# Kernel tuning notes

Measured on AMD Instinct MI355X. Metric: run time of the kernel, lower is better.

## Reference

```python
import jax, jax.numpy as jnp
import numpy as np

N, C, H, W = 4, 256, 32, 32
NH = 2                      # att_nhead
HD = C // NH                # 128 per-head dim
MAX_DIS = 7
WS = 2 * MAX_DIS + 1        # 15 window side
WW = WS * WS                # 225 window positions
T = (C / NH) ** 0.5


def _gather_idx(h, w):
    # idx[wpos, m]: flat index into zero-padded (h+14, w+14) grid of the
    # neighbor at window offset wpos for query pixel m (== F.unfold semantics)
    pw = w + 2 * MAX_DIS
    dy, dx = np.meshgrid(np.arange(WS), np.arange(WS), indexing='ij')
    ys, xs = np.meshgrid(np.arange(h), np.arange(w), indexing='ij')
    idx = (dy.reshape(-1, 1) + ys.reshape(1, -1)) * pw + (dx.reshape(-1, 1) + xs.reshape(1, -1))
    return jnp.asarray(idx, dtype=jnp.int32)  # [WW, h*w]


def setup_inputs() -> dict:
    key = jax.random.key(0)
    ks = jax.random.split(key, 14)
    s = 0.02
    return {
        'q': jax.random.normal(ks[0], (N, C, H, W), jnp.float32),
        'k': jax.random.normal(ks[1], (N, C, H, W), jnp.float32),
        'v': jax.random.normal(ks[2], (N, C, H, W), jnp.float32),
        'Wq': jax.random.normal(ks[3], (C, C), jnp.float32) * s,
        'bq': jnp.zeros((C,), jnp.float32),
        'Wk': jax.random.normal(ks[4], (C, C), jnp.float32) * s,
        'bk': jnp.zeros((C,), jnp.float32),
        'Wv': jax.random.normal(ks[5], (C, C), jnp.float32) * s,
        'bv': jnp.zeros((C,), jnp.float32),
        'Wrel': jax.random.normal(ks[6], (NH, WW, HD), jnp.float32) * s,   # grouped 1x1 conv
        'brel': jnp.zeros((NH * WW,), jnp.float32),
        'V_bias': jax.random.normal(ks[7], (NH, HD, WW), jnp.float32) * s,
        'Wfc': jax.random.normal(ks[8], (C, C), jnp.float32) * s,
        'bfc': jnp.zeros((C,), jnp.float32),
    }


def _conv1x1(x, Wt, b):
    return jnp.einsum('nchw,dc->ndhw', x, Wt) + b[None, :, None, None]


def reference(q, k, v, Wq, bq, Wk, bk, Wv, bv, Wrel, brel, V_bias, Wfc, bfc):
    n, c, h, w = q.shape
    hw = h * w
    idx = _gather_idx(h, w)                                   # [WW, hw]
    pad = ((0, 0), (0, 0), (0, 0), (MAX_DIS, MAX_DIS), (MAX_DIS, MAX_DIS))

    q = _conv1x1(q, Wq, bq)
    k = _conv1x1(k, Wk, bk)
    v = _conv1x1(v, Wv, bv)

    # grouped 1x1 conv: relative position logits, [n, NH, WW, hw]
    rel = jnp.einsum('ngcxy,gwc->ngwxy', q.reshape(n, NH, HD, h, w), Wrel)
    rel = rel + brel.reshape(NH, WW)[None, :, :, None, None]
    rel = rel.reshape(n, NH, WW, hw)

    qs = (q / T).reshape(n, NH, HD, hw)

    # unfold K via zero-pad + gather: [n, NH, HD, WW, hw]
    k_pad = jnp.pad(k.reshape(n, NH, HD, h, w), pad).reshape(n, NH, HD, -1)
    k_un = k_pad[..., idx]
    qk = jnp.einsum('ngcm,ngcwm->ngwm', qs, k_un) + rel

    # boundary mask: neighbor inside the original image
    valid = jnp.pad(jnp.ones((h, w), jnp.float32), MAX_DIS).reshape(-1)[idx] > 0
    qk = jnp.where(valid[None, None], qk, jnp.float32(-1e8))
    attn = jax.nn.softmax(qk, axis=2)                         # over window positions

    agg_bias = jnp.einsum('ngwm,gcw->mngc', attn, V_bias).reshape(hw, n, c)

    # local2global scatter + dense einsum == gather of zero-padded V
    v_pad = jnp.pad(v.reshape(n, NH, HD, h, w), pad).reshape(n, NH, HD, -1)
    v_un = v_pad[..., idx]                                    # [n, NH, HD, WW, hw]
    agg_value = jnp.einsum('ngwm,ngcwm->mngc', attn, v_un).reshape(hw, n, c)

    out = (agg_value + agg_bias) @ Wfc.T + bfc                # [hw, n, c]
    return out
```

## Files before the change

### kernel.cpp

```cpp
#include <hip/hip_runtime.h>
#include <math.h>


typedef __attribute__((ext_vector_type(8))) short short8;
typedef __attribute__((ext_vector_type(4))) short short4v;
typedef __attribute__((ext_vector_type(4))) float floatx4;

__device__ __forceinline__ short f2bf(float f) {
    unsigned u = __float_as_uint(f);
    unsigned r = (u + 0x7fffu + ((u >> 16) & 1u)) >> 16;
    return (short)r;
}
__device__ __forceinline__ float bf2f(short s) {
    return __uint_as_float(((unsigned)(unsigned short)s) << 16);
}

__global__ __launch_bounds__(256)
void conv_kernel(const float* __restrict__ q, const float* __restrict__ k,
                 const float* __restrict__ v,
                 const float* __restrict__ Wq, const float* __restrict__ Wk,
                 const float* __restrict__ Wv, const float* __restrict__ Wfc,
                 const float* __restrict__ Wrel,
                 short* __restrict__ Xhi, short* __restrict__ Xlo,
                 short* __restrict__ Whi, short* __restrict__ Wlo,
                 short* __restrict__ Wrh, short* __restrict__ Wrl)
{
    const int tid = threadIdx.x;
    const int z = blockIdx.z;
    const int lane = tid & 63;
    const int n16 = lane & 15, quad = lane >> 4;

    if (z < 12) {
        __shared__ float st[64 * 33];
        const int sel = z >> 2, batch = z & 3;
        const float* X = (sel == 0 ? q : sel == 1 ? k : v) + ((long)batch << 18);
        const int mb = blockIdx.x, kc = blockIdx.y;
#pragma unroll
        for (int it = 0; it < 8; ++it) {
            int e = tid + it * 256;
            int cc = e >> 6, mm = e & 63;
            st[mm * 33 + cc] = X[((long)(kc * 32 + cc) << 10) + mb * 64 + mm];
        }
        __syncthreads();
        const int mtl = tid >> 6;
        const int m = mtl * 16 + n16;
        short h[8], l[8];
#pragma unroll
        for (int j = 0; j < 8; ++j) {
            float f = st[m * 33 + quad * 8 + j];
            short hb = f2bf(f);
            h[j] = hb;
            l[j] = f2bf(f - bf2f(hb));
        }
        int mt16 = mb * 4 + mtl;
        long off = (long)z * 262144 + (((long)(mt16 * 8 + kc) * 64) + lane) * 8;
        *(short8*)(Xhi + off) = *(short8*)&h[0];
        *(short8*)(Xlo + off) = *(short8*)&l[0];
    } else if (z < 16) {
        if (tid >= 64) return;
        const int w = z - 12;
        const float* W = (w == 0 ? Wq : w == 1 ? Wk : w == 2 ? Wv : Wfc);
        const int dt = blockIdx.x, kc = blockIdx.y;
        const int d = dt * 16 + n16, cb = kc * 32 + quad * 8;
        float4 w0 = *(const float4*)&W[d * 256 + cb];
        float4 w1 = *(const float4*)&W[d * 256 + cb + 4];
        float f[8] = {w0.x, w0.y, w0.z, w0.w, w1.x, w1.y, w1.z, w1.w};
        short h[8], l[8];
#pragma unroll
        for (int j = 0; j < 8; ++j) {
            short hb = f2bf(f[j]);
            h[j] = hb;
            l[j] = f2bf(f[j] - bf2f(hb));
        }
        long off = (long)w * 65536 + (((long)(dt * 8 + kc) * 64) + lane) * 8;
        *(short8*)(Whi + off) = *(short8*)&h[0];
        *(short8*)(Wlo + off) = *(short8*)&l[0];
    } else {
        if (tid >= 64) return;
        const int g = z - 16;
        const int wt = blockIdx.x, kc = blockIdx.y;
        if (wt >= 15 || kc >= 4) return;
        const int w = wt * 16 + n16;
        const int cb = kc * 32 + quad * 8;
        float f[8] = {0.f, 0.f, 0.f, 0.f, 0.f, 0.f, 0.f, 0.f};
        if (w < 225) {
            float4 w0 = *(const float4*)&Wrel[(long)(g * 225 + w) * 128 + cb];
            float4 w1 = *(const float4*)&Wrel[(long)(g * 225 + w) * 128 + cb + 4];
            f[0] = w0.x; f[1] = w0.y; f[2] = w0.z; f[3] = w0.w;
            f[4] = w1.x; f[5] = w1.y; f[6] = w1.z; f[7] = w1.w;
        }
        short h[8], l[8];
#pragma unroll
        for (int j = 0; j < 8; ++j) {
            short hb = f2bf(f[j]);
            h[j] = hb;
            l[j] = f2bf(f[j] - bf2f(hb));
        }
        long off = (long)g * 30720 + (((long)(wt * 4 + kc) * 64) + lane) * 8;
        *(short8*)(Wrh + off) = *(short8*)&h[0];
        *(short8*)(Wrl + off) = *(short8*)&l[0];
    }
}

__global__ __launch_bounds__(256)
void mfma_proj(const short* __restrict__ Xhi, const short* __restrict__ Xlo,
               const short* __restrict__ Whi, const short* __restrict__ Wlo,
               const float* __restrict__ bq, const float* __restrict__ bk,
               const float* __restrict__ bv,
               short* __restrict__ qhi, short* __restrict__ qlo,
               short* __restrict__ khi, short* __restrict__ klo,
               float* __restrict__ vpad)
{
    __shared__ float tile[16 * 65];
    const int tid = threadIdx.x;
    const int wave = tid >> 6, lane = tid & 63;
    const int n16 = lane & 15, quad = lane >> 4;
    const int mt16 = blockIdx.x, db = blockIdx.y, z = blockIdx.z;
    const int sel = z >> 2, batch = z & 3;
    const int dt = db * 4 + wave;

    const short* Ah = Whi + (long)sel * 65536 + ((long)(dt * 8) * 64 + lane) * 8;
    const short* Al = Wlo + (long)sel * 65536 + ((long)(dt * 8) * 64 + lane) * 8;
    const short* Bh = Xhi + (long)z * 262144;
    const short* Bl = Xlo + (long)z * 262144;

    const float* bias = (sel == 0 ? bq : sel == 1 ? bk : bv);
    float4 bv4 = *(const float4*)&bias[dt * 16 + quad * 4];
    float bb[4] = {bv4.x, bv4.y, bv4.z, bv4.w};

    floatx4 acc = {0.f, 0.f, 0.f, 0.f};
#pragma unroll
    for (int kc = 0; kc < 8; ++kc) {
        short8 ahi = *(const short8*)(Ah + kc * 512);
        short8 alo = *(const short8*)(Al + kc * 512);
        long bo = ((long)(mt16 * 8 + kc) * 64 + lane) * 8;
        short8 bh = *(const short8*)(Bh + bo);
        short8 bl = *(const short8*)(Bl + bo);
        acc = __builtin_amdgcn_mfma_f32_16x16x32_bf16(ahi, bh, acc, 0, 0, 0);
        acc = __builtin_amdgcn_mfma_f32_16x16x32_bf16(ahi, bl, acc, 0, 0, 0);
        acc = __builtin_amdgcn_mfma_f32_16x16x32_bf16(alo, bh, acc, 0, 0, 0);
    }

    if (sel == 2) {
        const int m = mt16 * 16 + n16;
        float* Y = vpad + (long)batch * 393216;
        const int row = m >> 5, col = (m & 31) + 8;
#pragma unroll
        for (int r = 0; r < 4; ++r)
            Y[(long)(dt * 16 + quad * 4 + r) * 1536 + row * 48 + col] = acc[r] + bb[r];
        {
            const int prow = mt16 >> 1, side = mt16 & 1;
            const int ch_l = tid >> 2, f2 = (tid & 3) * 2;
            long po = (long)(db * 64 + ch_l) * 1536 + prow * 48 + side * 40 + f2;
            Y[po] = 0.f;
            Y[po + 1] = 0.f;
        }
        return;
    }

    const int cl = wave * 16 + quad * 4;
#pragma unroll
    for (int r = 0; r < 4; ++r)
        tile[n16 * 65 + cl + r] = acc[r] + bb[r];
    __syncthreads();

    const float scale = (sel == 1) ? 0.08838834764831845f : 1.0f;
    const int m_l = tid >> 4, c16 = (tid & 15) * 4;
    const int m = mt16 * 16 + m_l;
    const int cglob = db * 64 + c16;
    const int g = cglob >> 7, ch = cglob & 127;
    const long base = (((long)(batch * 2 + g) << 10) + m) * 128 + ch;
    short h[4], l[4];
#pragma unroll
    for (int j = 0; j < 4; ++j) {
        float f = tile[m_l * 65 + c16 + j] * scale;
        short hb = f2bf(f);
        h[j] = hb;
        l[j] = f2bf(f - bf2f(hb));
    }
    short* oh = sel ? khi : qhi;
    short* ol = sel ? klo : qlo;
    *(short4v*)(oh + base) = *(short4v*)&h[0];
    *(short4v*)(ol + base) = *(short4v*)&l[0];
}

__global__ __launch_bounds__(256)
void scores_pv(const short* __restrict__ qhi, const short* __restrict__ qlo,
               const short* __restrict__ khi, const short* __restrict__ klo,
               const short* __restrict__ Wrh, const short* __restrict__ Wrl,
               const float* __restrict__ brel,
               const float* __restrict__ vpad, const float* __restrict__ Vbias,
               short* __restrict__ AGhi, short* __restrict__ AGlo)
{
    __shared__ float qk[16 * 241];
    __shared__ float pa2[225 * 16];
    __shared__ float tile[16 * 133];
    __shared__ float invl[16];

    const int tid = threadIdx.x;
    const int wave = tid >> 6, lane = tid & 63;
    const int y  = blockIdx.x >> 1;
    const int xt = blockIdx.x & 1;
    const int bz = blockIdx.y;
    const int g = bz & 1;
    const int x0 = xt * 16;

    const int n16 = lane & 15, quad = lane >> 4;
    const long qbase = (((long)bz << 10) + y * 32 + x0 + n16) * 128 + quad * 8;
    short8 a_hi[4], a_lo[4];
#pragma unroll
    for (int ch = 0; ch < 4; ++ch) {
        a_hi[ch] = *(const short8*)(qhi + qbase + ch * 32);
        a_lo[ch] = *(const short8*)(qlo + qbase + ch * 32);
    }

    for (int wt = wave; wt < 15; wt += 4) {
        const short* Ah = Wrh + (long)g * 30720 + ((long)(wt * 4) * 64 + lane) * 8;
        const short* Al = Wrl + (long)g * 30720 + ((long)(wt * 4) * 64 + lane) * 8;
        floatx4 racc = {0.f, 0.f, 0.f, 0.f};
#pragma unroll
        for (int kc = 0; kc < 4; ++kc) {
            short8 whh = *(const short8*)(Ah + kc * 512);
            short8 wll = *(const short8*)(Al + kc * 512);
            racc = __builtin_amdgcn_mfma_f32_16x16x32_bf16(whh, a_hi[kc], racc, 0, 0, 0);
            racc = __builtin_amdgcn_mfma_f32_16x16x32_bf16(whh, a_lo[kc], racc, 0, 0, 0);
            racc = __builtin_amdgcn_mfma_f32_16x16x32_bf16(wll, a_hi[kc], racc, 0, 0, 0);
        }
#pragma unroll
        for (int r = 0; r < 4; ++r) {
            int w = wt * 16 + quad * 4 + r;
            if (w < 225) {
                int dy = w / 15, dx = w - dy * 15;
                qk[n16 * 241 + dy * 16 + dx] = racc[r] + brel[g * 225 + w];
            }
        }
    }
    __syncthreads();

    for (int e = tid; e < 16 * 241; e += 256) {
        int px = e / 241, idx = e - px * 241;
        int dy = idx >> 4, dx = idx & 15;
        int hy = y + dy - 7, hx = x0 + px + dx - 7;
        bool valid = (dx < 15) && (dy < 15) &&
                     (hy >= 0) && (hy < 32) && (hx >= 0) && (hx < 32);
        if (!valid) qk[e] = -1e8f;
    }
    __syncthreads();

    for (int dy = wave; dy < 15; dy += 4) {
        const int ky = y + dy - 7;
        if (ky < 0 || ky > 31) continue;
#pragma unroll
        for (int kxt = 0; kxt < 2; ++kxt) {
            const int kxg = x0 - 8 + kxt * 16 + n16;
            const long kb = (((long)bz << 10) + ky * 32 + kxg) * 128 + quad * 8;
            floatx4 acc = {0.f, 0.f, 0.f, 0.f};
#pragma unroll
            for (int ch = 0; ch < 4; ++ch) {
                short8 b_hi = *(const short8*)(khi + kb + ch * 32);
                short8 b_lo = *(const short8*)(klo + kb + ch * 32);
                acc = __builtin_amdgcn_mfma_f32_16x16x32_bf16(a_hi[ch], b_hi, acc, 0, 0, 0);
                acc = __builtin_amdgcn_mfma_f32_16x16x32_bf16(a_hi[ch], b_lo, acc, 0, 0, 0);
                acc = __builtin_amdgcn_mfma_f32_16x16x32_bf16(a_lo[ch], b_hi, acc, 0, 0, 0);
            }
            if (kxg >= 0 && kxg < 32) {
#pragma unroll
                for (int r = 0; r < 4; ++r) {
                    int m = quad * 4 + r;
                    int dx = kxg - (x0 + m) + 7;
                    if (dx >= 0 && dx < 15) {
                        int s = m * 241 + dy * 16 + dx;
                        qk[s] = qk[s] + acc[r];
                    }
                }
            }
        }
    }
    __syncthreads();

    {
        int px = tid >> 4, s = tid & 15;
        float mx = -3.0e38f;
        for (int w = s; w < 240; w += 16) mx = fmaxf(mx, qk[px * 241 + w]);
#pragma unroll
        for (int msk = 8; msk; msk >>= 1) mx = fmaxf(mx, __shfl_xor(mx, msk));
        float sum = 0.f;
        for (int w = s; w < 240; w += 16) {
            float p = __expf(qk[px * 241 + w] - mx);
            qk[px * 241 + w] = p;
            sum += p;
        }
#pragma unroll
        for (int msk = 8; msk; msk >>= 1) sum += __shfl_xor(sum, msk);
        if (s == 0) invl[px] = 1.0f / sum;
    }
    __syncthreads();

    for (int e = tid; e < 3600; e += 256) {
        int w = e >> 4, px = e & 15;
        int dy2 = w / 15, dx2 = w - dy2 * 15;
        pa2[w * 16 + px] = qk[px * 241 + dy2 * 16 + dx2] * invl[px];
    }
    __syncthreads();

    const int n = bz >> 1;
    const int chg2 = tid >> 2;
    const int xq   = tid & 3;
    const int c0   = chg2 * 2;
    const int xb   = x0 + xq * 4;
    const float* v0 = vpad + (long)bz * 196608 + (long)c0 * 1536;
    const float* v1 = v0 + 1536;
    const float* b0 = Vbias + (g * 128 + c0) * 225;
    const float* b1 = b0 + 225;

    float acc0[4] = {0.f, 0.f, 0.f, 0.f};
    float acc1[4] = {0.f, 0.f, 0.f, 0.f};

    for (int dy = 0; dy < 15; ++dy) {
        int hy = y + dy - 7;
        if (hy < 0 || hy > 31) continue;
        const float4* r0 = (const float4*)(v0 + hy * 48 + xb);
        const float4* r1 = (const float4*)(v1 + hy * 48 + xb);
        float wa[20], wb[20];
#pragma unroll
        for (int t = 0; t < 5; ++t) {
            float4 a = r0[t], b = r1[t];
            wa[4*t+0] = a.x; wa[4*t+1] = a.y; wa[4*t+2] = a.z; wa[4*t+3] = a.w;
            wb[4*t+0] = b.x; wb[4*t+1] = b.y; wb[4*t+2] = b.z; wb[4*t+3] = b.w;
        }
        const float* par = &pa2[dy * 15 * 16 + xq * 4];
        const float* vb0 = b0 + dy * 15;
        const float* vb1 = b1 + dy * 15;
#pragma unroll
        for (int dx = 0; dx < 15; ++dx) {
            float4 p4 = *(const float4*)&par[dx * 16];
            float ba = vb0[dx], bb = vb1[dx];
            acc0[0] += p4.x * (wa[1 + dx] + ba);
            acc0[1] += p4.y * (wa[2 + dx] + ba);
            acc0[2] += p4.z * (wa[3 + dx] + ba);
            acc0[3] += p4.w * (wa[4 + dx] + ba);
            acc1[0] += p4.x * (wb[1 + dx] + bb);
            acc1[1] += p4.y * (wb[2 + dx] + bb);
            acc1[2] += p4.z * (wb[3 + dx] + bb);
            acc1[3] += p4.w * (wb[4 + dx] + bb);
        }
    }

#pragma unroll
    for (int i = 0; i < 4; ++i) {
        tile[(xq * 4 + i) * 133 + c0 + 0] = acc0[i];
        tile[(xq * 4 + i) * 133 + c0 + 1] = acc1[i];
    }
    __syncthreads();

    const int sub = tid >> 6;
    short h[8], l[8];
#pragma unroll
    for (int j = 0; j < 8; ++j) {
        float f = tile[n16 * 133 + sub * 32 + quad * 8 + j];
        short hb = f2bf(f);
        h[j] = hb;
        l[j] = f2bf(f - bf2f(hb));
    }
    const int mt16 = y * 2 + xt;
    const int kc = g * 4 + sub;
    long off = (long)n * 262144 + (((long)(mt16 * 8 + kc) * 64) + lane) * 8;
    *(short8*)(AGhi + off) = *(short8*)&h[0];
    *(short8*)(AGlo + off) = *(short8*)&l[0];
}

__global__ __launch_bounds__(256)
void mfma_fc(const short* __restrict__ Ahi, const short* __restrict__ Alo,
             const short* __restrict__ Whi, const short* __restrict__ Wlo,
             const float* __restrict__ bfc, float* __restrict__ out)
{
    __shared__ float tile[16 * 68];
    const int tid = threadIdx.x;
    const int wave = tid >> 6, lane = tid & 63;
    const int n16 = lane & 15, quad = lane >> 4;
    const int mt16 = blockIdx.x, db = blockIdx.y, nz = blockIdx.z;
    const int dt = db * 4 + wave;

    const short* Ah = Whi + (long)3 * 65536 + ((long)(dt * 8) * 64 + lane) * 8;
    const short* Al = Wlo + (long)3 * 65536 + ((long)(dt * 8) * 64 + lane) * 8;
    const short* Bh = Ahi + (long)nz * 262144;
    const short* Bl = Alo + (long)nz * 262144;

    float4 bv4 = *(const float4*)&bfc[dt * 16 + quad * 4];
    float bb[4] = {bv4.x, bv4.y, bv4.z, bv4.w};

    floatx4 acc = {0.f, 0.f, 0.f, 0.f};
#pragma unroll
    for (int kc = 0; kc < 8; ++kc) {
        short8 ahi = *(const short8*)(Ah + kc * 512);
        short8 alo = *(const short8*)(Al + kc * 512);
        long bo = ((long)(mt16 * 8 + kc) * 64 + lane) * 8;
        short8 bh = *(const short8*)(Bh + bo);
        short8 bl = *(const short8*)(Bl + bo);
        acc = __builtin_amdgcn_mfma_f32_16x16x32_bf16(ahi, bh, acc, 0, 0, 0);
        acc = __builtin_amdgcn_mfma_f32_16x16x32_bf16(ahi, bl, acc, 0, 0, 0);
        acc = __builtin_amdgcn_mfma_f32_16x16x32_bf16(alo, bh, acc, 0, 0, 0);
    }

    const int dl = wave * 16 + quad * 4;
#pragma unroll
    for (int r = 0; r < 4; ++r)
        tile[n16 * 68 + dl + r] = acc[r] + bb[r];
    __syncthreads();

    const int mm = tid >> 4, d4 = (tid & 15) * 4;
    float4 o4 = *(const float4*)&tile[mm * 68 + d4];
    *(float4*)&out[(long)(mt16 * 16 + mm) * 1024 + nz * 256 + db * 64 + d4] = o4;
}

extern "C" void kernel_launch(void* const* d_in, const int* in_sizes, int n_in,
                              void* d_out, int out_size, void* d_ws, size_t ws_size,
                              hipStream_t stream)
{
    const float* q    = (const float*)d_in[0];
    const float* k    = (const float*)d_in[1];
    const float* v    = (const float*)d_in[2];
    const float* Wq   = (const float*)d_in[3];
    const float* bq   = (const float*)d_in[4];
    const float* Wk   = (const float*)d_in[5];
    const float* bk   = (const float*)d_in[6];
    const float* Wv   = (const float*)d_in[7];
    const float* bv   = (const float*)d_in[8];
    const float* Wrel = (const float*)d_in[9];
    const float* brel = (const float*)d_in[10];
    const float* Vb   = (const float*)d_in[11];
    const float* Wfc  = (const float*)d_in[12];
    const float* bfc  = (const float*)d_in[13];
    float* out = (float*)d_out;

    float* ws   = (float*)d_ws;
    float* vpad = ws + 2097152;
    short* qhi  = (short*)(ws + 6561792);
    short* qlo  = (short*)(ws + 7086080);
    short* khi  = (short*)(ws + 7610368);
    short* klo  = (short*)(ws + 8134656);
    short* Xhi  = (short*)(ws + 8658944);
    short* Xlo  = (short*)(ws + 10231808);
    short* Whi  = (short*)(ws + 11804672);
    short* Wlo  = (short*)(ws + 11935744);
    short* AGhi = (short*)(ws + 12066816);
    short* AGlo = (short*)(ws + 12591104);
    short* Wrh  = (short*)(ws + 13115392);
    short* Wrl  = (short*)(ws + 13146112);

    dim3 blk(256);

    conv_kernel<<<dim3(16, 8, 18), blk, 0, stream>>>(q, k, v, Wq, Wk, Wv, Wfc,
                                                     Wrel, Xhi, Xlo, Whi, Wlo,
                                                     Wrh, Wrl);

    mfma_proj<<<dim3(64, 4, 12), blk, 0, stream>>>(Xhi, Xlo, Whi, Wlo,
                                                   bq, bk, bv,
                                                   qhi, qlo, khi, klo, vpad);

    scores_pv<<<dim3(64, 8), blk, 0, stream>>>(qhi, qlo, khi, klo,
                                               Wrh, Wrl, brel,
                                               vpad, Vb, AGhi, AGlo);

    mfma_fc<<<dim3(64, 4, 4), blk, 0, stream>>>(AGhi, AGlo, Whi, Wlo, bfc, out);
}
```

Baseline: 169.9 us.

## Split scores_pv channel work across two blocks and alias shared memory

Doubles the scores_pv grid from 512 to 1024 blocks by splitting the 128 channels into two halves, each block computing one channel per thread instead of two. The grid is linearized with batch-head fastest. The qk and output tile shared buffers are aliased to cut LDS use and allow more resident blocks. The cost is that the QK scores, relative logits and softmax are now computed twice per pixel tile, once in each channel-half block.

```diff
diff --git a/kernel.cpp b/kernel.cpp
--- a/kernel.cpp
+++ b/kernel.cpp
@@ -192,16 +192,21 @@
                const float* __restrict__ vpad, const float* __restrict__ Vbias,
                short* __restrict__ AGhi, short* __restrict__ AGlo)
 {
-    __shared__ float qk[16 * 241];
-    __shared__ float pa2[225 * 16];
-    __shared__ float tile[16 * 133];
+    __shared__ __align__(16) float smem[16 * 241 + 225 * 16];
     __shared__ float invl[16];
+    float* qk   = smem;
+    float* pa2  = smem + 16 * 241;
+    float* tile = smem;
 
     const int tid = threadIdx.x;
     const int wave = tid >> 6, lane = tid & 63;
-    const int y  = blockIdx.x >> 1;
-    const int xt = blockIdx.x & 1;
-    const int bz = blockIdx.y;
+    const int lin = blockIdx.x;
+    const int bz  = lin & 7;
+    const int r2  = lin >> 3;
+    const int chh = r2 & 1;
+    const int yy  = r2 >> 1;
+    const int y   = yy >> 1;
+    const int xt  = yy & 1;
     const int g = bz & 1;
     const int x0 = xt * 16;
 
@@ -304,69 +309,59 @@
     __syncthreads();
 
     const int n = bz >> 1;
-    const int chg2 = tid >> 2;
-    const int xq   = tid & 3;
-    const int c0   = chg2 * 2;
-    const int xb   = x0 + xq * 4;
+    const int chg = tid >> 2;
+    const int xq  = tid & 3;
+    const int c0  = chh * 64 + chg;
+    const int xb  = x0 + xq * 4;
     const float* v0 = vpad + (long)bz * 196608 + (long)c0 * 1536;
-    const float* v1 = v0 + 1536;
     const float* b0 = Vbias + (g * 128 + c0) * 225;
-    const float* b1 = b0 + 225;
 
     float acc0[4] = {0.f, 0.f, 0.f, 0.f};
-    float acc1[4] = {0.f, 0.f, 0.f, 0.f};
 
     for (int dy = 0; dy < 15; ++dy) {
         int hy = y + dy - 7;
         if (hy < 0 || hy > 31) continue;
         const float4* r0 = (const float4*)(v0 + hy * 48 + xb);
-        const float4* r1 = (const float4*)(v1 + hy * 48 + xb);
-        float wa[20], wb[20];
+        float wa[20];
 #pragma unroll
         for (int t = 0; t < 5; ++t) {
-            float4 a = r0[t], b = r1[t];
+            float4 a = r0[t];
             wa[4*t+0] = a.x; wa[4*t+1] = a.y; wa[4*t+2] = a.z; wa[4*t+3] = a.w;
-            wb[4*t+0] = b.x; wb[4*t+1] = b.y; wb[4*t+2] = b.z; wb[4*t+3] = b.w;
         }
         const float* par = &pa2[dy * 15 * 16 + xq * 4];
         const float* vb0 = b0 + dy * 15;
-        const float* vb1 = b1 + dy * 15;
 #pragma unroll
         for (int dx = 0; dx < 15; ++dx) {
             float4 p4 = *(const float4*)&par[dx * 16];
-            float ba = vb0[dx], bb = vb1[dx];
+            float ba = vb0[dx];
             acc0[0] += p4.x * (wa[1 + dx] + ba);
             acc0[1] += p4.y * (wa[2 + dx] + ba);
             acc0[2] += p4.z * (wa[3 + dx] + ba);
             acc0[3] += p4.w * (wa[4 + dx] + ba);
-            acc1[0] += p4.x * (wb[1 + dx] + bb);
-            acc1[1] += p4.y * (wb[2 + dx] + bb);
-            acc1[2] += p4.z * (wb[3 + dx] + bb);
-            acc1[3] += p4.w * (wb[4 + dx] + bb);
-        }
-    }
-
-#pragma unroll
-    for (int i = 0; i < 4; ++i) {
-        tile[(xq * 4 + i) * 133 + c0 + 0] = acc0[i];
-        tile[(xq * 4 + i) * 133 + c0 + 1] = acc1[i];
-    }
+        }
+    }
+
+#pragma unroll
+    for (int i = 0; i < 4; ++i)
+        tile[(xq * 4 + i) * 68 + chg] = acc0[i];
     __syncthreads();
 
     const int sub = tid >> 6;
-    short h[8], l[8];
-#pragma unroll
-    for (int j = 0; j < 8; ++j) {
-        float f = tile[n16 * 133 + sub * 32 + quad * 8 + j];
-        short hb = f2bf(f);
-        h[j] = hb;
-        l[j] = f2bf(f - bf2f(hb));
-    }
-    const int mt16 = y * 2 + xt;
-    const int kc = g * 4 + sub;
-    long off = (long)n * 262144 + (((long)(mt16 * 8 + kc) * 64) + lane) * 8;
-    *(short8*)(AGhi + off) = *(short8*)&h[0];
-    *(short8*)(AGlo + off) = *(short8*)&l[0];
+    if (sub < 2) {
+        short h[8], l[8];
+#pragma unroll
+        for (int j = 0; j < 8; ++j) {
+            float f = tile[n16 * 68 + sub * 32 + quad * 8 + j];
+            short hb = f2bf(f);
+            h[j] = hb;
+            l[j] = f2bf(f - bf2f(hb));
+        }
+        const int mt16 = y * 2 + xt;
+        const int kc = g * 4 + chh * 2 + sub;
+        long off = (long)n * 262144 + (((long)(mt16 * 8 + kc) * 64) + lane) * 8;
+        *(short8*)(AGhi + off) = *(short8*)&h[0];
+        *(short8*)(AGlo + off) = *(short8*)&l[0];
+    }
 }
 
 __global__ __launch_bounds__(256)
@@ -458,9 +453,9 @@
                                                    bq, bk, bv,
                                                    qhi, qlo, khi, klo, vpad);
 
-    scores_pv<<<dim3(64, 8), blk, 0, stream>>>(qhi, qlo, khi, klo,
-                                               Wrh, Wrl, brel,
-                                               vpad, Vb, AGhi, AGlo);
+    scores_pv<<<dim3(1024), blk, 0, stream>>>(qhi, qlo, khi, klo,
+                                              Wrh, Wrl, brel,
+                                              vpad, Vb, AGhi, AGlo);
 
     mfma_fc<<<dim3(64, 4, 4), blk, 0, stream>>>(AGhi, AGlo, Whi, Wlo, bfc, out);
 }
```

After: 167.5 us. No clear change (-1.4%).
